# Kernel tuning notes

Hardware: AMD Instinct MI355X
Metric: run time of the kernel (lower is better)

## Reference

```python
import jax, jax.numpy as jnp
import numpy as np

NEG_BIG = -1.0e9


def setup_inputs() -> dict:
    key = jax.random.key(0)
    ks = jax.random.split(key, 8)
    B, N, D = 4, 384, 256
    s = 1.0 / np.sqrt(D)
    return {
        "q": jax.random.normal(ks[0], (B, N, D), dtype=jnp.float32),
        "k": jax.random.normal(ks[1], (B, N, D), dtype=jnp.float32),
        "v": jax.random.normal(ks[2], (B, N, D), dtype=jnp.float32),
        "mask": jax.random.randint(ks[3], (B, 1, N, N), 0, 2, dtype=jnp.int32),
        "Wq": jax.random.normal(ks[4], (D, D), dtype=jnp.float32) * s,
        "bq": jnp.zeros((D,), dtype=jnp.float32),
        "Wk": jax.random.normal(ks[5], (D, D), dtype=jnp.float32) * s,
        "bk": jnp.zeros((D,), dtype=jnp.float32),
        "Wv": jax.random.normal(ks[6], (D, D), dtype=jnp.float32) * s,
        "bv": jnp.zeros((D,), dtype=jnp.float32),
    }


def reference(q, k, v, mask, Wq, bq, Wk, bk, Wv, bv):
    # Dense projections
    query = q @ Wq + bq   # [B, N, D]
    key_p = k @ Wk + bk   # [B, M, D]
    value = v @ Wv + bv   # [B, M, D]
    # Per-channel outer-product scores: [B, D, N, M]
    score = jnp.einsum('bnd,bmd->bdnm', query, key_p)
    score = score + mask.astype(score.dtype) * NEG_BIG  # mask broadcasts [B,1,N,M]
    weights = jnp.tanh(score)
    # Per-channel weighted sum back to [B, N, D]
    out = jnp.einsum('bdnm,bmd->bnd', weights, value)
    return out
```

## Files before the change

### kernel.cpp

```cpp
#include <hip/hip_runtime.h>

#define DD 256
#define NN 384
#define BB 4
#define BN (BB * NN)
#define MSPLIT 8
#define MCHUNK (NN / MSPLIT)
#define ROWS 8
#define KSPLIT 4
#define KCH (DD / KSPLIT)
#define QP (BN * DD)
#define PLANE (3 * QP)

constexpr float TWO_LOG2E = 2.8853900817779268f;
constexpr float MASK_X    = -1.0e9f * 2.8853900817779268f;

__global__ __launch_bounds__(128) void proj_kernel(
    const float* __restrict__ q,  const float* __restrict__ k,  const float* __restrict__ v,
    const float* __restrict__ Wq, const float* __restrict__ Wk, const float* __restrict__ Wv,
    float* __restrict__ Pp)
{
    const int tid   = threadIdx.x;
    const int row0  = blockIdx.x * 4;
    const int which = blockIdx.y;
    const int k0    = blockIdx.z * KCH;

    const float* X = (which == 0) ? q  : (which == 1) ? k  : v;
    const float* W = (which == 0) ? Wq : (which == 1) ? Wk : Wv;

    __shared__ float xs[4][KCH];
    {
        const int e0 = tid;
        xs[e0 >> 6][e0 & 63] = X[(size_t)(row0 + (e0 >> 6)) * DD + k0 + (e0 & 63)];
        const int e1 = tid + 128;
        xs[e1 >> 6][e1 & 63] = X[(size_t)(row0 + (e1 >> 6)) * DD + k0 + (e1 & 63)];
    }
    __syncthreads();

    const float* Wp = W + (size_t)k0 * DD + tid * 2;

    float2 a0{0.f,0.f}, a1{0.f,0.f}, a2{0.f,0.f}, a3{0.f,0.f};

    #pragma unroll 2
    for (int g = 0; g < KCH; g += 4) {
        const float2 w0 = *reinterpret_cast<const float2*>(Wp + (size_t)(g + 0) * DD);
        const float2 w1 = *reinterpret_cast<const float2*>(Wp + (size_t)(g + 1) * DD);
        const float2 w2 = *reinterpret_cast<const float2*>(Wp + (size_t)(g + 2) * DD);
        const float2 w3 = *reinterpret_cast<const float2*>(Wp + (size_t)(g + 3) * DD);
        const float4 x0 = *reinterpret_cast<const float4*>(&xs[0][g]);
        const float4 x1 = *reinterpret_cast<const float4*>(&xs[1][g]);
        const float4 x2 = *reinterpret_cast<const float4*>(&xs[2][g]);
        const float4 x3 = *reinterpret_cast<const float4*>(&xs[3][g]);

        a0.x = fmaf(x0.x, w0.x, a0.x); a0.y = fmaf(x0.x, w0.y, a0.y);
        a1.x = fmaf(x1.x, w0.x, a1.x); a1.y = fmaf(x1.x, w0.y, a1.y);
        a2.x = fmaf(x2.x, w0.x, a2.x); a2.y = fmaf(x2.x, w0.y, a2.y);
        a3.x = fmaf(x3.x, w0.x, a3.x); a3.y = fmaf(x3.x, w0.y, a3.y);

        a0.x = fmaf(x0.y, w1.x, a0.x); a0.y = fmaf(x0.y, w1.y, a0.y);
        a1.x = fmaf(x1.y, w1.x, a1.x); a1.y = fmaf(x1.y, w1.y, a1.y);
        a2.x = fmaf(x2.y, w1.x, a2.x); a2.y = fmaf(x2.y, w1.y, a2.y);
        a3.x = fmaf(x3.y, w1.x, a3.x); a3.y = fmaf(x3.y, w1.y, a3.y);

        a0.x = fmaf(x0.z, w2.x, a0.x); a0.y = fmaf(x0.z, w2.y, a0.y);
        a1.x = fmaf(x1.z, w2.x, a1.x); a1.y = fmaf(x1.z, w2.y, a1.y);
        a2.x = fmaf(x2.z, w2.x, a2.x); a2.y = fmaf(x2.z, w2.y, a2.y);
        a3.x = fmaf(x3.z, w2.x, a3.x); a3.y = fmaf(x3.z, w2.y, a3.y);

        a0.x = fmaf(x0.w, w3.x, a0.x); a0.y = fmaf(x0.w, w3.y, a0.y);
        a1.x = fmaf(x1.w, w3.x, a1.x); a1.y = fmaf(x1.w, w3.y, a1.y);
        a2.x = fmaf(x2.w, w3.x, a2.x); a2.y = fmaf(x2.w, w3.y, a2.y);
        a3.x = fmaf(x3.w, w3.x, a3.x); a3.y = fmaf(x3.w, w3.y, a3.y);
    }

    float* o = Pp + (size_t)blockIdx.z * PLANE + (size_t)which * QP
             + (size_t)row0 * DD + tid * 2;
    *reinterpret_cast<float2*>(o + 0 * DD) = a0;
    *reinterpret_cast<float2*>(o + 1 * DD) = a1;
    *reinterpret_cast<float2*>(o + 2 * DD) = a2;
    *reinterpret_cast<float2*>(o + 3 * DD) = a3;
}

__global__ __launch_bounds__(256) void preduce_kernel(
    const float* __restrict__ Pp,
    const float* __restrict__ bq, const float* __restrict__ bk, const float* __restrict__ bv,
    float* __restrict__ Qout, float* __restrict__ KVout)
{
    const int which = blockIdx.y;
    const int i = blockIdx.x * 256 + threadIdx.x;
    const float* p = Pp + (size_t)which * QP + i;
    const float s = (p[0] + p[(size_t)PLANE]) + (p[2 * (size_t)PLANE] + p[3 * (size_t)PLANE]);
    const int d = i & 255;
    if (which == 0)      Qout[i]          = s + bq[d];
    else if (which == 1) KVout[2 * i]     = (s + bk[d]) * TWO_LOG2E;
    else                 KVout[2 * i + 1] = s + bv[d];
}

__global__ __launch_bounds__(256) void mhsa_kernel(
    const float* __restrict__ Q, const float* __restrict__ KV,
    const int* __restrict__ mask, float* __restrict__ outp)
{
    const int tid = threadIdx.x;
    const int b   = blockIdx.y;
    const int n0  = blockIdx.x * ROWS;
    const int m0  = blockIdx.z * MCHUNK;

    __shared__ float mf[MCHUNK][ROWS];
    for (int idx = tid; idx < MCHUNK * ROWS; idx += 256) {
        const int m = idx % MCHUNK;
        const int j = idx / MCHUNK;
        mf[m][j] = mask[(size_t)(b * NN + n0 + j) * NN + (m0 + m)] ? MASK_X : 0.0f;
    }
    __syncthreads();

    const float* Qp = Q + (size_t)(b * NN + n0) * DD + tid;
    float qv0 = Qp[0 * DD], qv1 = Qp[1 * DD], qv2 = Qp[2 * DD], qv3 = Qp[3 * DD];
    float qv4 = Qp[4 * DD], qv5 = Qp[5 * DD], qv6 = Qp[6 * DD], qv7 = Qp[7 * DD];

    const float2* kvp = reinterpret_cast<const float2*>(KV)
                      + (size_t)b * NN * DD + (size_t)m0 * DD + tid;

    float acc0 = 0.f, acc1 = 0.f, acc2 = 0.f, acc3 = 0.f;
    float acc4 = 0.f, acc5 = 0.f, acc6 = 0.f, acc7 = 0.f, vsum = 0.f;

#define TANH1(ACC, XV, T2) \
    ACC = fmaf(T2, __builtin_amdgcn_rcpf(__builtin_amdgcn_exp2f(XV) + 1.0f), ACC);

#define COMP(KVV, MLOC)                                                        \
    {                                                                          \
        const float4 ma = *reinterpret_cast<const float4*>(&mf[MLOC][0]);      \
        const float4 mb = *reinterpret_cast<const float4*>(&mf[MLOC][4]);      \
        const float kk = (KVV).x, vv = (KVV).y;                                \
        const float t2 = -2.0f * vv;                                           \
        vsum += vv;                                                            \
        TANH1(acc0, fmaf(qv0, kk, ma.x), t2)                                   \
        TANH1(acc1, fmaf(qv1, kk, ma.y), t2)                                   \
        TANH1(acc2, fmaf(qv2, kk, ma.z), t2)                                   \
        TANH1(acc3, fmaf(qv3, kk, ma.w), t2)                                   \
        TANH1(acc4, fmaf(qv4, kk, mb.x), t2)                                   \
        TANH1(acc5, fmaf(qv5, kk, mb.y), t2)                                   \
        TANH1(acc6, fmaf(qv6, kk, mb.z), t2)                                   \
        TANH1(acc7, fmaf(qv7, kk, mb.w), t2)                                   \
    }

#define LOADG(B0, B1, B2, B3, M0)                \
    B0 = kvp[(size_t)((M0) + 0) * DD];           \
    B1 = kvp[(size_t)((M0) + 1) * DD];           \
    B2 = kvp[(size_t)((M0) + 2) * DD];           \
    B3 = kvp[(size_t)((M0) + 3) * DD];

    float2 A0, A1, A2, A3, B0, B1, B2, B3;
    LOADG(A0, A1, A2, A3, 0)
    LOADG(B0, B1, B2, B3, 4)

    for (int mg = 0; mg < MCHUNK; mg += 8) {
        COMP(A0, mg + 0) COMP(A1, mg + 1) COMP(A2, mg + 2) COMP(A3, mg + 3)
        LOADG(A0, A1, A2, A3, mg + 8)
        COMP(B0, mg + 4) COMP(B1, mg + 5) COMP(B2, mg + 6) COMP(B3, mg + 7)
        LOADG(B0, B1, B2, B3, mg + 12)
    }
#undef COMP
#undef TANH1
#undef LOADG

    float* po = outp + (size_t)blockIdx.z * QP + (size_t)(b * NN + n0) * DD + tid;
    po[0 * DD] = acc0 + vsum; po[1 * DD] = acc1 + vsum;
    po[2 * DD] = acc2 + vsum; po[3 * DD] = acc3 + vsum;
    po[4 * DD] = acc4 + vsum; po[5 * DD] = acc5 + vsum;
    po[6 * DD] = acc6 + vsum; po[7 * DD] = acc7 + vsum;
}

__global__ __launch_bounds__(256) void reduce8_kernel(
    const float* __restrict__ part, float* __restrict__ out)
{
    const int i = blockIdx.x * 256 + threadIdx.x;
    float s0 = part[i + 0 * (size_t)QP] + part[i + 1 * (size_t)QP];
    float s1 = part[i + 2 * (size_t)QP] + part[i + 3 * (size_t)QP];
    float s2 = part[i + 4 * (size_t)QP] + part[i + 5 * (size_t)QP];
    float s3 = part[i + 6 * (size_t)QP] + part[i + 7 * (size_t)QP];
    out[i] = (s0 + s1) + (s2 + s3);
}

extern "C" void kernel_launch(void* const* d_in, const int* in_sizes, int n_in,
                              void* d_out, int out_size, void* d_ws, size_t ws_size,
                              hipStream_t stream) {
    const float* q    = (const float*)d_in[0];
    const float* k    = (const float*)d_in[1];
    const float* v    = (const float*)d_in[2];
    const int*   mask = (const int*)  d_in[3];
    const float* Wq   = (const float*)d_in[4];
    const float* bq   = (const float*)d_in[5];
    const float* Wk   = (const float*)d_in[6];
    const float* bk   = (const float*)d_in[7];
    const float* Wv   = (const float*)d_in[8];
    const float* bv   = (const float*)d_in[9];
    float* out = (float*)d_out;

    float* Qws  = (float*)d_ws;
    float* KVws = Qws  + (size_t)QP;
    float* Pp   = KVws + (size_t)2 * QP;
    float* Pm   = Pp   + (size_t)KSPLIT * PLANE;

    proj_kernel<<<dim3(BN / 4, 3, KSPLIT), 128, 0, stream>>>(
        q, k, v, Wq, Wk, Wv, Pp);

    preduce_kernel<<<dim3(QP / 256, 3), 256, 0, stream>>>(
        Pp, bq, bk, bv, Qws, KVws);

    mhsa_kernel<<<dim3(NN / ROWS, BB, MSPLIT), 256, 0, stream>>>(
        Qws, KVws, mask, Pm);

    reduce8_kernel<<<dim3(QP / 256), 256, 0, stream>>>(Pm, out);
}
```

Measured before the change: 137.7 us.

## Retile projection to 8 rows with float4 weights and halve attention row tile

The projection kernel now gives each block 8 rows, with each wave computing 4 rows by 4 columns. Weights are read as float4 and x is stored transposed in shared memory so one float4 load feeds 16 FMAs. The attention kernel drops from 8 to 4 query rows per block, doubling the grid and cutting register use, and adds occupancy hints to the launch bounds. The aim is more waves in flight on the tanh/exp-bound attention kernel, at the cost of reading the KV stream twice as often.

Result: faster. 130.7 us (-5.1%).

```diff
diff --git a/kernel.cpp b/kernel.cpp
--- a/kernel.cpp
+++ b/kernel.cpp
@@ -6,7 +6,6 @@
 #define BN (BB * NN)
 #define MSPLIT 8
 #define MCHUNK (NN / MSPLIT)
-#define ROWS 8
 #define KSPLIT 4
 #define KCH (DD / KSPLIT)
 #define QP (BN * DD)
@@ -15,70 +14,55 @@
 constexpr float TWO_LOG2E = 2.8853900817779268f;
 constexpr float MASK_X    = -1.0e9f * 2.8853900817779268f;
 
-__global__ __launch_bounds__(128) void proj_kernel(
+__global__ __launch_bounds__(128, 6) void proj_kernel(
     const float* __restrict__ q,  const float* __restrict__ k,  const float* __restrict__ v,
     const float* __restrict__ Wq, const float* __restrict__ Wk, const float* __restrict__ Wv,
     float* __restrict__ Pp)
 {
     const int tid   = threadIdx.x;
-    const int row0  = blockIdx.x * 4;
+    const int lane  = tid & 63;
+    const int wv    = tid >> 6;
+    const int row0  = blockIdx.x * 8;
     const int which = blockIdx.y;
     const int k0    = blockIdx.z * KCH;
 
     const float* X = (which == 0) ? q  : (which == 1) ? k  : v;
     const float* W = (which == 0) ? Wq : (which == 1) ? Wk : Wv;
 
-    __shared__ float xs[4][KCH];
-    {
-        const int e0 = tid;
-        xs[e0 >> 6][e0 & 63] = X[(size_t)(row0 + (e0 >> 6)) * DD + k0 + (e0 & 63)];
-        const int e1 = tid + 128;
-        xs[e1 >> 6][e1 & 63] = X[(size_t)(row0 + (e1 >> 6)) * DD + k0 + (e1 & 63)];
+    __shared__ float xs[KCH][8];
+    #pragma unroll
+    for (int e = tid; e < 8 * KCH; e += 128) {
+        const int r  = e >> 6;
+        const int kk = e & 63;
+        xs[kk][r] = X[(size_t)(row0 + r) * DD + k0 + kk];
     }
     __syncthreads();
 
-    const float* Wp = W + (size_t)k0 * DD + tid * 2;
+    const int r4 = wv * 4;
+    const float* Wp = W + (size_t)k0 * DD + lane * 4;
 
-    float2 a0{0.f,0.f}, a1{0.f,0.f}, a2{0.f,0.f}, a3{0.f,0.f};
+    float4 a0 = make_float4(0.f,0.f,0.f,0.f), a1 = a0, a2 = a0, a3 = a0;
 
     #pragma unroll 2
-    for (int g = 0; g < KCH; g += 4) {
-        const float2 w0 = *reinterpret_cast<const float2*>(Wp + (size_t)(g + 0) * DD);
-        const float2 w1 = *reinterpret_cast<const float2*>(Wp + (size_t)(g + 1) * DD);
-        const float2 w2 = *reinterpret_cast<const float2*>(Wp + (size_t)(g + 2) * DD);
-        const float2 w3 = *reinterpret_cast<const float2*>(Wp + (size_t)(g + 3) * DD);
-        const float4 x0 = *reinterpret_cast<const float4*>(&xs[0][g]);
-        const float4 x1 = *reinterpret_cast<const float4*>(&xs[1][g]);
-        const float4 x2 = *reinterpret_cast<const float4*>(&xs[2][g]);
-        const float4 x3 = *reinterpret_cast<const float4*>(&xs[3][g]);
-
-        a0.x = fmaf(x0.x, w0.x, a0.x); a0.y = fmaf(x0.x, w0.y, a0.y);
-        a1.x = fmaf(x1.x, w0.x, a1.x); a1.y = fmaf(x1.x, w0.y, a1.y);
-        a2.x = fmaf(x2.x, w0.x, a2.x); a2.y = fmaf(x2.x, w0.y, a2.y);
-        a3.x = fmaf(x3.x, w0.x, a3.x); a3.y = fmaf(x3.x, w0.y, a3.y);
-
-        a0.x = fmaf(x0.y, w1.x, a0.x); a0.y = fmaf(x0.y, w1.y, a0.y);
-        a1.x = fmaf(x1.y, w1.x, a1.x); a1.y = fmaf(x1.y, w1.y, a1.y);
-        a2.x = fmaf(x2.y, w1.x, a2.x); a2.y = fmaf(x2.y, w1.y, a2.y);
-        a3.x = fmaf(x3.y, w1.x, a3.x); a3.y = fmaf(x3.y, w1.y, a3.y);
-
-        a0.x = fmaf(x0.z, w2.x, a0.x); a0.y = fmaf(x0.z, w2.y, a0.y);
-        a1.x = fmaf(x1.z, w2.x, a1.x); a1.y = fmaf(x1.z, w2.y, a1.y);
-        a2.x = fmaf(x2.z, w2.x, a2.x); a2.y = fmaf(x2.z, w2.y, a2.y);
-        a3.x = fmaf(x3.z, w2.x, a3.x); a3.y = fmaf(x3.z, w2.y, a3.y);
-
-        a0.x = fmaf(x0.w, w3.x, a0.x); a0.y = fmaf(x0.w, w3.y, a0.y);
-        a1.x = fmaf(x1.w, w3.x, a1.x); a1.y = fmaf(x1.w, w3.y, a1.y);
-        a2.x = fmaf(x2.w, w3.x, a2.x); a2.y = fmaf(x2.w, w3.y, a2.y);
-        a3.x = fmaf(x3.w, w3.x, a3.x); a3.y = fmaf(x3.w, w3.y, a3.y);
+    for (int kk = 0; kk < KCH; ++kk) {
+        const float4 w4 = *reinterpret_cast<const float4*>(Wp + (size_t)kk * DD);
+        const float4 xr = *reinterpret_cast<const float4*>(&xs[kk][r4]);
+        a0.x = fmaf(xr.x, w4.x, a0.x); a0.y = fmaf(xr.x, w4.y, a0.y);
+        a0.z = fmaf(xr.x, w4.z, a0.z); a0.w = fmaf(xr.x, w4.w, a0.w);
+        a1.x = fmaf(xr.y, w4.x, a1.x); a1.y = fmaf(xr.y, w4.y, a1.y);
+        a1.z = fmaf(xr.y, w4.z, a1.z); a1.w = fmaf(xr.y, w4.w, a1.w);
+        a2.x = fmaf(xr.z, w4.x, a2.x); a2.y = fmaf(xr.z, w4.y, a2.y);
+        a2.z = fmaf(xr.z, w4.z, a2.z); a2.w = fmaf(xr.z, w4.w, a2.w);
+        a3.x = fmaf(xr.w, w4.x, a3.x); a3.y = fmaf(xr.w, w4.y, a3.y);
+        a3.z = fmaf(xr.w, w4.z, a3.z); a3.w = fmaf(xr.w, w4.w, a3.w);
     }
 
     float* o = Pp + (size_t)blockIdx.z * PLANE + (size_t)which * QP
-             + (size_t)row0 * DD + tid * 2;
-    *reinterpret_cast<float2*>(o + 0 * DD) = a0;
-    *reinterpret_cast<float2*>(o + 1 * DD) = a1;
-    *reinterpret_cast<float2*>(o + 2 * DD) = a2;
-    *reinterpret_cast<float2*>(o + 3 * DD) = a3;
+             + (size_t)(row0 + r4) * DD + lane * 4;
+    *reinterpret_cast<float4*>(o + 0 * DD) = a0;
+    *reinterpret_cast<float4*>(o + 1 * DD) = a1;
+    *reinterpret_cast<float4*>(o + 2 * DD) = a2;
+    *reinterpret_cast<float4*>(o + 3 * DD) = a3;
 }
 
 __global__ __launch_bounds__(256) void preduce_kernel(
@@ -96,51 +80,44 @@
     else                 KVout[2 * i + 1] = s + bv[d];
 }
 
-__global__ __launch_bounds__(256) void mhsa_kernel(
+__global__ __launch_bounds__(256, 8) void mhsa_kernel(
     const float* __restrict__ Q, const float* __restrict__ KV,
     const int* __restrict__ mask, float* __restrict__ outp)
 {
     const int tid = threadIdx.x;
     const int b   = blockIdx.y;
-    const int n0  = blockIdx.x * ROWS;
+    const int n0  = blockIdx.x * 4;
     const int m0  = blockIdx.z * MCHUNK;
 
-    __shared__ float mf[MCHUNK][ROWS];
-    for (int idx = tid; idx < MCHUNK * ROWS; idx += 256) {
-        const int m = idx % MCHUNK;
-        const int j = idx / MCHUNK;
+    __shared__ float mf[MCHUNK][4];
+    if (tid < MCHUNK * 4) {
+        const int m = tid % MCHUNK;
+        const int j = tid / MCHUNK;
         mf[m][j] = mask[(size_t)(b * NN + n0 + j) * NN + (m0 + m)] ? MASK_X : 0.0f;
     }
     __syncthreads();
 
     const float* Qp = Q + (size_t)(b * NN + n0) * DD + tid;
-    float qv0 = Qp[0 * DD], qv1 = Qp[1 * DD], qv2 = Qp[2 * DD], qv3 = Qp[3 * DD];
-    float qv4 = Qp[4 * DD], qv5 = Qp[5 * DD], qv6 = Qp[6 * DD], qv7 = Qp[7 * DD];
+    const float qv0 = Qp[0 * DD], qv1 = Qp[1 * DD], qv2 = Qp[2 * DD], qv3 = Qp[3 * DD];
 
     const float2* kvp = reinterpret_cast<const float2*>(KV)
                       + (size_t)b * NN * DD + (size_t)m0 * DD + tid;
 
-    float acc0 = 0.f, acc1 = 0.f, acc2 = 0.f, acc3 = 0.f;
-    float acc4 = 0.f, acc5 = 0.f, acc6 = 0.f, acc7 = 0.f, vsum = 0.f;
+    float acc0 = 0.f, acc1 = 0.f, acc2 = 0.f, acc3 = 0.f, vsum = 0.f;
 
 #define TANH1(ACC, XV, T2) \
     ACC = fmaf(T2, __builtin_amdgcn_rcpf(__builtin_amdgcn_exp2f(XV) + 1.0f), ACC);
 
 #define COMP(KVV, MLOC)                                                        \
     {                                                                          \
-        const float4 ma = *reinterpret_cast<const float4*>(&mf[MLOC][0]);      \
-        const float4 mb = *reinterpret_cast<const float4*>(&mf[MLOC][4]);      \
+        const float4 m4 = *reinterpret_cast<const float4*>(&mf[MLOC][0]);      \
         const float kk = (KVV).x, vv = (KVV).y;                                \
         const float t2 = -2.0f * vv;                                           \
         vsum += vv;                                                            \
-        TANH1(acc0, fmaf(qv0, kk, ma.x), t2)                                   \
-        TANH1(acc1, fmaf(qv1, kk, ma.y), t2)                                   \
-        TANH1(acc2, fmaf(qv2, kk, ma.z), t2)                                   \
-        TANH1(acc3, fmaf(qv3, kk, ma.w), t2)                                   \
-        TANH1(acc4, fmaf(qv4, kk, mb.x), t2)                                   \
-        TANH1(acc5, fmaf(qv5, kk, mb.y), t2)                                   \
-        TANH1(acc6, fmaf(qv6, kk, mb.z), t2)                                   \
-        TANH1(acc7, fmaf(qv7, kk, mb.w), t2)                                   \
+        TANH1(acc0, fmaf(qv0, kk, m4.x), t2)                                   \
+        TANH1(acc1, fmaf(qv1, kk, m4.y), t2)                                   \
+        TANH1(acc2, fmaf(qv2, kk, m4.z), t2)                                   \
+        TANH1(acc3, fmaf(qv3, kk, m4.w), t2)                                   \
     }
 
 #define LOADG(B0, B1, B2, B3, M0)                \
@@ -166,8 +143,6 @@
     float* po = outp + (size_t)blockIdx.z * QP + (size_t)(b * NN + n0) * DD + tid;
     po[0 * DD] = acc0 + vsum; po[1 * DD] = acc1 + vsum;
     po[2 * DD] = acc2 + vsum; po[3 * DD] = acc3 + vsum;
-    po[4 * DD] = acc4 + vsum; po[5 * DD] = acc5 + vsum;
-    po[6 * DD] = acc6 + vsum; po[7 * DD] = acc7 + vsum;
 }
 
 __global__ __launch_bounds__(256) void reduce8_kernel(
@@ -201,13 +176,13 @@
     float* Pp   = KVws + (size_t)2 * QP;
     float* Pm   = Pp   + (size_t)KSPLIT * PLANE;
 
-    proj_kernel<<<dim3(BN / 4, 3, KSPLIT), 128, 0, stream>>>(
+    proj_kernel<<<dim3(BN / 8, 3, KSPLIT), 128, 0, stream>>>(
         q, k, v, Wq, Wk, Wv, Pp);
 
     preduce_kernel<<<dim3(QP / 256, 3), 256, 0, stream>>>(
         Pp, bq, bk, bv, Qws, KVws);
 
-    mhsa_kernel<<<dim3(NN / ROWS, BB, MSPLIT), 256, 0, stream>>>(
+    mhsa_kernel<<<dim3(NN / 4, BB, MSPLIT), 256, 0, stream>>>(
         Qws, KVws, mask, Pm);
 
     reduce8_kernel<<<dim3(QP / 256), 256, 0, stream>>>(Pm, out);
```
